# Kernel tuning notes

Measured on AMD Instinct MI355X. Metric: run time of the kernel, lower is better.

## Reference

```python
import jax, jax.numpy as jnp
import numpy as np

N_NODES = 50000
N_EDGES_UND = 400000
N_GRAPHS = 128
LATENT = 64
OUT_DIM = 64
NODE_F = 64
EDGE_F = 32
MAX_LV = 3


def setup_inputs() -> dict:
    key = jax.random.key(0)
    ks = jax.random.split(key, 12)
    rng = np.random.default_rng(0)
    # Build consistent directed edge list: each undirected pair (u,v) yields
    # directed edges e (u->v) and e+E_und (v->u); rev maps each to its twin.
    u = rng.integers(0, N_NODES, size=N_EDGES_UND)
    v = rng.integers(0, N_NODES, size=N_EDGES_UND)
    src = jnp.asarray(np.concatenate([u, v]), dtype=jnp.int32)
    dst = jnp.asarray(np.concatenate([v, u]), dtype=jnp.int32)
    e = np.arange(N_EDGES_UND)
    rev = jnp.asarray(np.concatenate([e + N_EDGES_UND, e]), dtype=jnp.int32)
    graph_ids = jnp.sort(jax.random.randint(ks[0], (N_NODES,), 0, N_GRAPHS)).astype(jnp.int32)
    s = 0.05
    return {
        'node_feat': jax.random.normal(ks[1], (N_NODES, NODE_F), jnp.float32),
        'edge_feat': jax.random.normal(ks[2], (2 * N_EDGES_UND, EDGE_F), jnp.float32),
        'src': src, 'dst': dst, 'rev': rev,
        'graph_ids': graph_ids, 'n_graphs': N_GRAPHS,
        'Wn': jax.random.normal(ks[3], (NODE_F, LATENT), jnp.float32) * s,
        'bn': jnp.zeros((LATENT,), jnp.float32),
        'We': jax.random.normal(ks[4], (EDGE_F, LATENT), jnp.float32) * s,
        'be': jnp.zeros((LATENT,), jnp.float32),
        'Wc': jax.random.normal(ks[5], (LATENT, LATENT), jnp.float32) * s,
        'bc': jnp.zeros((LATENT,), jnp.float32),
        'Wo': jax.random.normal(ks[6], (LATENT, OUT_DIM), jnp.float32) * s,
        'bo': jnp.zeros((OUT_DIM,), jnp.float32),
    }


def reference(node_feat, edge_feat, src, dst, rev, graph_ids, n_graphs,
              Wn, bn, We, be, Wc, bc, Wo, bo):
    n_nodes = node_feat.shape[0]
    # w_n2l / w_e2l
    input_node_linear = node_feat @ Wn + bn                  # [N, D]
    input_edge_linear = edge_feat @ We + be                  # [E, D]
    # n2e spmm: each directed edge gathers its source node's row
    input_message = input_edge_linear + input_node_linear[src]  # [E, D]
    cur = jax.nn.relu(input_message)
    # loopy BP: e2e spmm = (sum of messages into src node) - reverse-edge message
    for _ in range(MAX_LV):
        node_agg = jax.ops.segment_sum(cur, dst, num_segments=n_nodes)  # [N, D]
        e2epool = node_agg[src] - cur[rev]                              # [E, D]
        cur = jax.nn.relu(e2epool @ Wc + bc + input_message)
    # e2n spmm: sum incoming edge messages per node
    e2npool = jax.ops.segment_sum(cur, dst, num_segments=n_nodes)       # [N, D]
    hidden_msg = jax.nn.relu(e2npool)
    reluact = jax.nn.relu(hidden_msg @ Wo + bo)                         # [N, out]
    # subg spmm: sum node outputs per graph
    y = jax.ops.segment_sum(reluact, graph_ids, num_segments=n_graphs)  # [G, out]
    return jax.nn.relu(y)
```

## Files before the change

### kernel.cpp

```cpp
#include <hip/hip_runtime.h>


#define NN 50000
#define NE 800000
#define NG 128
#define D 64
#define LDE 36
#define LDW 66
#define LDO 72

typedef unsigned short u16;
typedef unsigned int u32;
typedef __bf16 bf16x8 __attribute__((ext_vector_type(8)));
typedef float f32x4 __attribute__((ext_vector_type(4)));

__device__ __forceinline__ float b2f(u16 u){ u32 x=((u32)u)<<16; float f; __builtin_memcpy(&f,&x,4); return f; }
__device__ __forceinline__ u16 f2b(float f){ u32 x; __builtin_memcpy(&x,&f,4); x += 0x7fffu + ((x>>16)&1u); return (u16)(x>>16); }
__device__ __forceinline__ u32 pack2(float a, float b){ return (u32)f2b(a) | ((u32)f2b(b)<<16); }
__device__ __forceinline__ void unpack8(uint4 v, float* o){
  o[0]=b2f((u16)(v.x&0xffffu)); o[1]=b2f((u16)(v.x>>16));
  o[2]=b2f((u16)(v.y&0xffffu)); o[3]=b2f((u16)(v.y>>16));
  o[4]=b2f((u16)(v.z&0xffffu)); o[5]=b2f((u16)(v.z>>16));
  o[6]=b2f((u16)(v.w&0xffffu)); o[7]=b2f((u16)(v.w>>16));
}

__global__ __launch_bounds__(256) void k_prep(const float* __restrict__ Wc, const float* __restrict__ We,
                                              u16* __restrict__ wcB, u16* __restrict__ weB){
  int i = blockIdx.x*256 + threadIdx.x;
  if (i < 4096){
    int nt = i>>10, r = i&1023;
    int h = r>>9, r2 = r&511;
    int j = r2>>3, kk = r2&7;
    int row = nt*16 + (j&15);
    int k = h*32 + (j>>4)*8 + kk;
    wcB[i] = f2b(Wc[k*D + row]);
  }
  int t = i - 4096;
  if (t >= 0 && t < 2048){
    int nt = t>>9, r = t&511;
    int j = r>>3, kk = r&7;
    int row = nt*16 + (j&15);
    int k = (j>>4)*8 + kk;
    weB[t] = f2b(We[k*D + row]);
  }
}

template<int ZERO>
__global__ __launch_bounds__(256) void k_cvt(const float* __restrict__ srcv, u16* __restrict__ dstb,
                                             float* __restrict__ zbuf){
  size_t i = (size_t)(blockIdx.x*256 + threadIdx.x)*4;
  float4 v = *(const float4*)(srcv + i);
  *(uint2*)(dstb + i) = make_uint2(pack2(v.x,v.y), pack2(v.z,v.w));
  if (ZERO) *(float4*)(zbuf + i) = make_float4(0.f,0.f,0.f,0.f);
}

__global__ __launch_bounds__(256) void k_inl(const float* __restrict__ nf, const float* __restrict__ Wn,
                                             const float* __restrict__ bn, u16* __restrict__ inlb){
  __shared__ float w[D*D];
  for (int i=threadIdx.x;i<D*D;i+=256) w[i]=Wn[i];
  __syncthreads();
  const int d = threadIdx.x&63;
  const int n = blockIdx.x*4 + (threadIdx.x>>6);
  if (n>=NN) return;
  float v = bn[d];
  const float* row = nf + (size_t)n*D;
  #pragma unroll 8
  for (int k=0;k<D;k++) v += row[k]*w[k*D+d];
  inlb[(size_t)n*D+d] = f2b(v);
}

__global__ __launch_bounds__(256) void k_imf2(const float* __restrict__ ef, const u16* __restrict__ weB,
        const float* __restrict__ be, const u16* __restrict__ inlb, const int* __restrict__ srcP,
        const int* __restrict__ eP, const int* __restrict__ nodeP, const u16* __restrict__ wcB,
        u16* __restrict__ imP, u16* __restrict__ revOut, float* __restrict__ naW_out){
  __shared__ __align__(16) u16 efs[64*LDE];
  __shared__ float osf[64*68];
  __shared__ __align__(16) u16 xs[64*LDW];
  __shared__ __align__(16) u16 osb[64*LDO];
  __shared__ int nid[64];
  const int t = threadIdx.x;
  const int lane = t&63, w = t>>6;
  const size_t sbase = (size_t)blockIdx.x*64;
  if (lane < 16) nid[w*16 + lane] = nodeP[sbase + w*16 + lane];
  {
    int r=t>>2, k0=(t&3)*8;
    const int e = eP[sbase + r];
    const float* p = ef + (size_t)e*32 + k0;
    float4 v0=*(const float4*)p, v1=*(const float4*)(p+4);
    *(uint4*)&efs[r*LDE+k0] = make_uint4(pack2(v0.x,v0.y),pack2(v0.z,v0.w),pack2(v1.x,v1.y),pack2(v1.z,v1.w));
  }
  {
    int q=lane>>4, mr=lane&15, rowb=w*16;
    bf16x8 A = *(const bf16x8*)&efs[(rowb+mr)*LDE + q*8];
    #pragma unroll
    for (int nt=0;nt<4;nt++){
      bf16x8 B = *(const bf16x8*)(weB + nt*512 + lane*8);
      f32x4 acc = {0.f,0.f,0.f,0.f};
      acc = __builtin_amdgcn_mfma_f32_16x16x32_bf16(A,B,acc,0,0,0);
      #pragma unroll
      for (int r=0;r<4;r++) osf[(rowb+q*4+r)*68 + nt*16+mr] = acc[r];
    }
  }
  {
    int r=t>>2, d0=(t&3)*16;
    const size_t slot = sbase + r;
    const int s = srcP[slot];
    const u16* ip = inlb + (size_t)s*D + d0;
    uint4 iv0 = *(const uint4*)ip, iv1 = *(const uint4*)(ip+8);
    float il[16]; unpack8(iv0,il); unpack8(iv1,il+8);
    float x[16];
    #pragma unroll
    for (int j=0;j<16;j++) x[j] = osf[r*68 + d0 + j] + be[d0+j] + il[j];
    uint4 p0 = make_uint4(pack2(x[0],x[1]),pack2(x[2],x[3]),pack2(x[4],x[5]),pack2(x[6],x[7]));
    uint4 p1 = make_uint4(pack2(x[8],x[9]),pack2(x[10],x[11]),pack2(x[12],x[13]),pack2(x[14],x[15]));
    u16* op = imP + slot*D + d0;
    *(uint4*)op = p0; *(uint4*)(op+8) = p1;
    #pragma unroll
    for (int j=0;j<16;j++) x[j] = x[j]>0.f ? x[j] : 0.f;
    uint4 q0 = make_uint4(pack2(x[0],x[1]),pack2(x[2],x[3]),pack2(x[4],x[5]),pack2(x[6],x[7]));
    uint4 q1 = make_uint4(pack2(x[8],x[9]),pack2(x[10],x[11]),pack2(x[12],x[13]),pack2(x[14],x[15]));
    u16* qd = &xs[r*LDW + d0];
    *(uint4*)qd = q0; *(uint4*)(qd+8) = q1;
  }
  {
    const int q = lane>>4, mr = lane&15;
    const int rowb = w*16;
    bf16x8 A0 = *(const bf16x8*)&xs[(rowb+mr)*LDW + q*8];
    bf16x8 A1 = *(const bf16x8*)&xs[(rowb+mr)*LDW + 32 + q*8];
    #pragma unroll
    for (int nt=0;nt<4;nt++){
      bf16x8 B0 = *(const bf16x8*)(wcB + nt*1024 + lane*8);
      bf16x8 B1 = *(const bf16x8*)(wcB + nt*1024 + 512 + lane*8);
      f32x4 acc = {0.f,0.f,0.f,0.f};
      acc = __builtin_amdgcn_mfma_f32_16x16x32_bf16(A0,B0,acc,0,0,0);
      acc = __builtin_amdgcn_mfma_f32_16x16x32_bf16(A1,B1,acc,0,0,0);
      #pragma unroll
      for (int r=0;r<4;r++) osb[(rowb+q*4+r)*LDO + nt*16 + mr] = f2b(acc[r]);
    }
    const int lr = lane>>2, cc = lane&3;
    u16* gp = revOut + (sbase + rowb + lr)*D + cc*16;
    *(uint4*)gp     = *(const uint4*)&osb[(rowb+lr)*LDO + cc*16];
    *(uint4*)(gp+8) = *(const uint4*)&osb[(rowb+lr)*LDO + cc*16 + 8];
    float acc = 0.f;
    int curn = nid[rowb];
    #pragma unroll 4
    for (int i=0;i<16;++i){
      int n = nid[rowb+i];
      if (n != curn){
        atomicAdd(&naW_out[(size_t)curn*D + lane], acc);
        curn = n; acc = 0.f;
      }
      acc += b2f(osb[(rowb+i)*LDO + lane]);
    }
    atomicAdd(&naW_out[(size_t)curn*D + lane], acc);
  }
}

__global__ __launch_bounds__(256) void k_iter1(const u16* __restrict__ imP, const u16* __restrict__ revIn,
      const u16* __restrict__ naWb, const u16* __restrict__ wcB, const float* __restrict__ bc,
      const int* __restrict__ srcP, const int* __restrict__ prevP, const int* __restrict__ nodeP,
      u16* __restrict__ revOut, float* __restrict__ naW_out){
  __shared__ __align__(16) u16 xs[64*LDW];
  __shared__ __align__(16) u16 os[64*LDO];
  __shared__ int nid[64];
  const int t = threadIdx.x;
  const int lane = t&63, w = t>>6;
  const size_t sbase = (size_t)blockIdx.x*64;
  if (lane < 16) nid[w*16 + lane] = nodeP[sbase + w*16 + lane];
  {
    const int e = t>>2, d0 = (t&3)*16;
    const size_t slot = sbase + e;
    const u16* ip = imP + slot*D + d0;
    uint4 r0 = *(const uint4*)ip, r1 = *(const uint4*)(ip+8);
    float x[16]; unpack8(r0,x); unpack8(r1,x+8);
    const int sp = srcP[slot];
    const int tw = prevP[slot];
    const u16* cp = revIn + (size_t)tw*D + d0;
    uint4 c0=*(const uint4*)cp, c1=*(const uint4*)(cp+8);
    const u16* np_ = naWb + (size_t)sp*D + d0;
    uint4 n0=*(const uint4*)np_, n1=*(const uint4*)(np_+8);
    float cv[16], nv[16];
    unpack8(c0,cv); unpack8(c1,cv+8);
    unpack8(n0,nv); unpack8(n1,nv+8);
    #pragma unroll
    for (int j=0;j<16;j++){ x[j] += nv[j] - cv[j] + bc[d0+j]; x[j] = x[j]>0.f ? x[j] : 0.f; }
    uint4 p0 = make_uint4(pack2(x[0],x[1]),pack2(x[2],x[3]),pack2(x[4],x[5]),pack2(x[6],x[7]));
    uint4 p1 = make_uint4(pack2(x[8],x[9]),pack2(x[10],x[11]),pack2(x[12],x[13]),pack2(x[14],x[15]));
    u16* qd = &xs[e*LDW + d0];
    *(uint4*)qd = p0; *(uint4*)(qd+8) = p1;
  }
  {
    const int q = lane>>4, mr = lane&15;
    const int rowb = w*16;
    bf16x8 A0 = *(const bf16x8*)&xs[(rowb+mr)*LDW + q*8];
    bf16x8 A1 = *(const bf16x8*)&xs[(rowb+mr)*LDW + 32 + q*8];
    #pragma unroll
    for (int nt=0;nt<4;nt++){
      bf16x8 B0 = *(const bf16x8*)(wcB + nt*1024 + lane*8);
      bf16x8 B1 = *(const bf16x8*)(wcB + nt*1024 + 512 + lane*8);
      f32x4 acc = {0.f,0.f,0.f,0.f};
      acc = __builtin_amdgcn_mfma_f32_16x16x32_bf16(A0,B0,acc,0,0,0);
      acc = __builtin_amdgcn_mfma_f32_16x16x32_bf16(A1,B1,acc,0,0,0);
      #pragma unroll
      for (int r=0;r<4;r++) os[(rowb+q*4+r)*LDO + nt*16 + mr] = f2b(acc[r]);
    }
    const int lr = lane>>2, cc = lane&3;
    u16* gp = revOut + (sbase + rowb + lr)*D + cc*16;
    *(uint4*)gp     = *(const uint4*)&os[(rowb+lr)*LDO + cc*16];
    *(uint4*)(gp+8) = *(const uint4*)&os[(rowb+lr)*LDO + cc*16 + 8];
    float acc = 0.f;
    int curn = nid[rowb];
    #pragma unroll 4
    for (int i=0;i<16;++i){
      int n = nid[rowb+i];
      if (n != curn){
        atomicAdd(&naW_out[(size_t)curn*D + lane], acc);
        curn = n; acc = 0.f;
      }
      acc += b2f(os[(rowb+i)*LDO + lane]);
    }
    atomicAdd(&naW_out[(size_t)curn*D + lane], acc);
  }
}

__global__ __launch_bounds__(256) void k_last(const u16* __restrict__ imP, const u16* __restrict__ revIn,
      const u16* __restrict__ naWb, const float* __restrict__ bc,
      const int* __restrict__ srcP, const int* __restrict__ prevP, const int* __restrict__ nodeP,
      float* __restrict__ e2n){
  __shared__ __align__(16) u16 xs[64*LDW];
  __shared__ int nid[64];
  const int t = threadIdx.x;
  const int lane = t&63, w = t>>6;
  const size_t sbase = (size_t)blockIdx.x*64;
  if (lane < 16) nid[w*16+lane] = nodeP[sbase + w*16 + lane];
  {
    const int e = t>>2, d0 = (t&3)*16;
    const size_t slot = sbase + e;
    const u16* ip = imP + slot*D + d0;
    uint4 r0 = *(const uint4*)ip, r1 = *(const uint4*)(ip+8);
    float x[16]; unpack8(r0,x); unpack8(r1,x+8);
    const int sp = srcP[slot];
    const int tw = prevP[slot];
    const u16* cp = revIn + (size_t)tw*D + d0;
    uint4 c0 = *(const uint4*)cp, c1 = *(const uint4*)(cp+8);
    const u16* np_ = naWb + (size_t)sp*D + d0;
    uint4 n0 = *(const uint4*)np_, n1 = *(const uint4*)(np_+8);
    float cv[16], nv[16];
    unpack8(c0,cv); unpack8(c1,cv+8);
    unpack8(n0,nv); unpack8(n1,nv+8);
    #pragma unroll
    for (int j=0;j<16;j++){ x[j] += nv[j] - cv[j] + bc[d0+j]; x[j] = x[j]>0.f ? x[j] : 0.f; }
    uint4 p0 = make_uint4(pack2(x[0],x[1]),pack2(x[2],x[3]),pack2(x[4],x[5]),pack2(x[6],x[7]));
    uint4 p1 = make_uint4(pack2(x[8],x[9]),pack2(x[10],x[11]),pack2(x[12],x[13]),pack2(x[14],x[15]));
    u16* qd = &xs[e*LDW + d0];
    *(uint4*)qd = p0; *(uint4*)(qd+8) = p1;
  }
  {
    float acc = 0.f;
    int curn = nid[w*16];
    #pragma unroll 4
    for (int i=0;i<16;++i){
      int n = nid[w*16+i];
      if (n != curn){
        atomicAdd(&e2n[(size_t)curn*D + lane], acc);
        curn = n; acc = 0.f;
      }
      acc += b2f(xs[(w*16+i)*LDW + lane]);
    }
    atomicAdd(&e2n[(size_t)curn*D + lane], acc);
  }
}

__global__ void k_hist(const int* __restrict__ dst, int* __restrict__ cnt){
  int e = blockIdx.x*256 + threadIdx.x;
  atomicAdd(&cnt[dst[e]], 1);
}
__global__ __launch_bounds__(1024) void k_scan1(const int* __restrict__ cnt, int* __restrict__ outv,
                                                int* __restrict__ bsums, int n){
  __shared__ int sh[1024];
  int i = blockIdx.x*1024 + threadIdx.x;
  int v = (i<n)? cnt[i] : 0;
  sh[threadIdx.x]=v;
  __syncthreads();
  for (int off=1; off<1024; off<<=1){
    int tv = (threadIdx.x>=(unsigned)off)? sh[threadIdx.x-off] : 0;
    __syncthreads();
    sh[threadIdx.x] += tv;
    __syncthreads();
  }
  if (i<n) outv[i] = sh[threadIdx.x] - v;
  if (threadIdx.x==1023) bsums[blockIdx.x] = sh[1023];
}
__global__ __launch_bounds__(1024) void k_scan3(int* __restrict__ off, int* __restrict__ cur,
                                                const int* __restrict__ bsums, int n){
  __shared__ int spref;
  if (threadIdx.x < 64){
    int v = ((int)threadIdx.x < (int)blockIdx.x) ? bsums[threadIdx.x] : 0;
    #pragma unroll
    for (int o=1;o<64;o<<=1) v += __shfl_xor(v, o, 64);
    if (threadIdx.x==0) spref = v;
  }
  __syncthreads();
  int i = blockIdx.x*1024 + threadIdx.x;
  if (i<n){ int v = off[i] + spref; off[i]=v; cur[i]=v; }
}
__global__ void k_fill(const int* __restrict__ dst, const int* __restrict__ src,
                       int* __restrict__ cur, int* __restrict__ perm,
                       int* __restrict__ srcP, int* __restrict__ nodeP, int* __restrict__ eP){
  int e = blockIdx.x*256 + threadIdx.x;
  int d = dst[e];
  int pos = atomicAdd(&cur[d], 1);
  perm[e] = pos;
  srcP[pos] = src[e];
  nodeP[pos] = d;
  eP[pos] = e;
}
__global__ void k_prev(const int* __restrict__ rev, const int* __restrict__ perm, int* __restrict__ prevP){
  int e = blockIdx.x*256 + threadIdx.x;
  prevP[perm[e]] = perm[rev[e]];
}

__global__ __launch_bounds__(256) void k_final(const float* __restrict__ e2n, const float* __restrict__ Wo,
                                               const float* __restrict__ bo, const int* __restrict__ gid,
                                               float* __restrict__ yacc){
  __shared__ float w[D*D];
  for (int i=threadIdx.x;i<D*D;i+=256) w[i]=Wo[i];
  __syncthreads();
  const int d = threadIdx.x&63, sub = threadIdx.x>>6;
  const int n0 = blockIdx.x*32 + sub*8;
  const float bod = bo[d];
  float acc=0.f; int curg=-1;
  for (int i=0;i<8;i++){
    int n=n0+i;
    if (n>=NN) break;
    int g = gid[n];
    if (g!=curg){ if (curg>=0) atomicAdd(&yacc[curg*D+d], acc); curg=g; acc=0.f; }
    float v=bod;
    const float* er = e2n + (size_t)n*D;
    #pragma unroll 8
    for (int k=0;k<D;k++){ float h=er[k]; h = h>0.f?h:0.f; v += h*w[k*D+d]; }
    acc += (v>0.f ? v : 0.f);
  }
  if (curg>=0) atomicAdd(&yacc[curg*D+d], acc);
}
__global__ void k_out(const float* __restrict__ yacc, float* __restrict__ outp){
  int i = blockIdx.x*256 + threadIdx.x;
  if (i<NG*D){ float v=yacc[i]; outp[i]= v>0.f?v:0.f; }
}

static constexpr size_t SZ_E   = (size_t)NE*D*2;
static constexpr size_t SZ_NF4 = (size_t)NN*D*4;
static constexpr size_t SZ_NB  = (size_t)NN*D*2;
static constexpr size_t OFF_IMP  = 0;
static constexpr size_t OFF_RVA  = SZ_E;
static constexpr size_t OFF_RVB  = 2*SZ_E;
static constexpr size_t OFF_CCUR = 3*SZ_E;
static constexpr size_t OFF_NA0  = OFF_CCUR + 200064;
static constexpr size_t OFF_NA1  = OFF_NA0 + SZ_NF4;
static constexpr size_t OFF_E2N  = OFF_NA1 + SZ_NF4;
static constexpr size_t OFF_YACC = OFF_E2N + SZ_NF4;
static constexpr size_t ZERO_SZ  = 200064 + 3*SZ_NF4 + (size_t)NG*D*4;
static constexpr size_t OFF_NAB  = OFF_YACC + (size_t)NG*D*4;
static constexpr size_t OFF_INL  = OFF_NAB + SZ_NB;
static constexpr size_t OFF_COFF = OFF_INL + SZ_NB;
static constexpr size_t OFF_PERM = OFF_COFF + 200064;
static constexpr size_t OFF_SRCP = OFF_PERM + (size_t)NE*4;
static constexpr size_t OFF_PRVP = OFF_SRCP + (size_t)NE*4;
static constexpr size_t OFF_NODP = OFF_PRVP + (size_t)NE*4;
static constexpr size_t OFF_EP   = OFF_NODP + (size_t)NE*4;
static constexpr size_t OFF_BS   = OFF_EP + (size_t)NE*4;
static constexpr size_t OFF_WCT  = OFF_BS + 256;
static constexpr size_t OFF_WET  = OFF_WCT + 8192;

extern "C" void kernel_launch(void* const* d_in, const int* in_sizes, int n_in,
                              void* d_out, int out_size, void* d_ws, size_t ws_size,
                              hipStream_t stream) {
  const float* node_feat = (const float*)d_in[0];
  const float* edge_feat = (const float*)d_in[1];
  const int*   src       = (const int*)d_in[2];
  const int*   dst       = (const int*)d_in[3];
  const int*   rev       = (const int*)d_in[4];
  const int*   gid       = (const int*)d_in[5];
  const float* Wn = (const float*)d_in[7];
  const float* bn = (const float*)d_in[8];
  const float* We = (const float*)d_in[9];
  const float* be = (const float*)d_in[10];
  const float* Wc = (const float*)d_in[11];
  const float* bc = (const float*)d_in[12];
  const float* Wo = (const float*)d_in[13];
  const float* bo = (const float*)d_in[14];

  char* ws = (char*)d_ws;
  u16*   imP     = (u16*)(ws + OFF_IMP);
  u16*   revA    = (u16*)(ws + OFF_RVA);
  u16*   revB    = (u16*)(ws + OFF_RVB);
  float* naW0    = (float*)(ws + OFF_NA0);
  float* naW1    = (float*)(ws + OFF_NA1);
  float* e2n     = (float*)(ws + OFF_E2N);
  float* yacc    = (float*)(ws + OFF_YACC);
  u16*   naWb    = (u16*)(ws + OFF_NAB);
  u16*   inlb    = (u16*)(ws + OFF_INL);
  int*   csr_off = (int*)(ws + OFF_COFF);
  int*   csr_cur = (int*)(ws + OFF_CCUR);
  int*   perm    = (int*)(ws + OFF_PERM);
  int*   srcP    = (int*)(ws + OFF_SRCP);
  int*   prevP   = (int*)(ws + OFF_PRVP);
  int*   nodeP   = (int*)(ws + OFF_NODP);
  int*   eP      = (int*)(ws + OFF_EP);
  int*   bsums   = (int*)(ws + OFF_BS);
  u16*   wcB     = (u16*)(ws + OFF_WCT);
  u16*   weB     = (u16*)(ws + OFF_WET);

  hipMemsetAsync(ws + OFF_CCUR, 0, ZERO_SZ, stream);

  k_hist <<<NE/256, 256, 0, stream>>>(dst, csr_cur);
  k_scan1<<<49, 1024, 0, stream>>>(csr_cur, csr_off, bsums, NN);
  k_scan3<<<49, 1024, 0, stream>>>(csr_off, csr_cur, bsums, NN);
  k_fill <<<NE/256, 256, 0, stream>>>(dst, src, csr_cur, perm, srcP, nodeP, eP);
  k_prev <<<NE/256, 256, 0, stream>>>(rev, perm, prevP);

  k_prep<<<24, 256, 0, stream>>>(Wc, We, wcB, weB);
  k_inl <<<NN/4, 256, 0, stream>>>(node_feat, Wn, bn, inlb);

  k_imf2<<<NE/64, 256, 0, stream>>>(edge_feat, weB, be, inlb, srcP, eP, nodeP, wcB, imP, revA, naW0);

  k_cvt<0><<<3125, 256, 0, stream>>>(naW0, naWb, (float*)nullptr);
  k_iter1<<<NE/64, 256, 0, stream>>>(imP, revA, naWb, wcB, bc, srcP, prevP, nodeP, revB, naW1);
  k_cvt<1><<<3125, 256, 0, stream>>>(naW1, naWb, naW0);
  k_iter1<<<NE/64, 256, 0, stream>>>(imP, revB, naWb, wcB, bc, srcP, prevP, nodeP, revA, naW0);
  k_cvt<0><<<3125, 256, 0, stream>>>(naW0, naWb, (float*)nullptr);
  k_last<<<NE/64, 256, 0, stream>>>(imP, revA, naWb, bc, srcP, prevP, nodeP, e2n);

  k_final<<<(NN+31)/32, 256, 0, stream>>>(e2n, Wo, bo, gid, yacc);
  k_out<<<(NG*D)/256, 256, 0, stream>>>(yacc, (float*)d_out);
}
```

Before: 697.3 us.

## Scatter reverse-edge messages at write time so consumers read them coalesced

Each producer kernel now writes its per-edge Wc-projected message to the reverse edge's slot via prevP, so the next iteration reads revIn at its own slot with coalesced loads instead of a random gather. The random access moves from the read side to the write side, where stores can be fire-and-forget. k_imf2 also packs its shared buffers into per-wave aliased regions to cut LDS use and raise occupancy. The risk is that scattered 32-byte stores are less efficient than coalesced ones.

```diff
diff --git a/kernel.cpp b/kernel.cpp
--- a/kernel.cpp
+++ b/kernel.cpp
@@ -8,6 +8,7 @@
 #define LDE 36
 #define LDW 66
 #define LDO 72
+#define PW 6464
 
 typedef unsigned short u16;
 typedef unsigned int u32;
@@ -71,38 +72,41 @@
 
 __global__ __launch_bounds__(256) void k_imf2(const float* __restrict__ ef, const u16* __restrict__ weB,
         const float* __restrict__ be, const u16* __restrict__ inlb, const int* __restrict__ srcP,
-        const int* __restrict__ eP, const int* __restrict__ nodeP, const u16* __restrict__ wcB,
+        const int* __restrict__ eP, const int* __restrict__ nodeP, const int* __restrict__ prevP,
+        const u16* __restrict__ wcB,
         u16* __restrict__ imP, u16* __restrict__ revOut, float* __restrict__ naW_out){
-  __shared__ __align__(16) u16 efs[64*LDE];
-  __shared__ float osf[64*68];
-  __shared__ __align__(16) u16 xs[64*LDW];
-  __shared__ __align__(16) u16 osb[64*LDO];
+  __shared__ __align__(16) char buf[4*PW];
   __shared__ int nid[64];
   const int t = threadIdx.x;
   const int lane = t&63, w = t>>6;
   const size_t sbase = (size_t)blockIdx.x*64;
+  char* wb = buf + w*PW;
+  float* osf = (float*)wb;
+  u16*   osb = (u16*)wb;
+  u16*   efs = (u16*)(wb + 4352);
+  u16*   xs  = (u16*)(wb + 4352);
   if (lane < 16) nid[w*16 + lane] = nodeP[sbase + w*16 + lane];
   {
-    int r=t>>2, k0=(t&3)*8;
+    int r=t>>2, lr=r&15, k0=(t&3)*8;
     const int e = eP[sbase + r];
     const float* p = ef + (size_t)e*32 + k0;
     float4 v0=*(const float4*)p, v1=*(const float4*)(p+4);
-    *(uint4*)&efs[r*LDE+k0] = make_uint4(pack2(v0.x,v0.y),pack2(v0.z,v0.w),pack2(v1.x,v1.y),pack2(v1.z,v1.w));
-  }
-  {
-    int q=lane>>4, mr=lane&15, rowb=w*16;
-    bf16x8 A = *(const bf16x8*)&efs[(rowb+mr)*LDE + q*8];
+    *(uint4*)&efs[lr*LDE+k0] = make_uint4(pack2(v0.x,v0.y),pack2(v0.z,v0.w),pack2(v1.x,v1.y),pack2(v1.z,v1.w));
+  }
+  {
+    int q=lane>>4, mr=lane&15;
+    bf16x8 A = *(const bf16x8*)&efs[mr*LDE + q*8];
     #pragma unroll
     for (int nt=0;nt<4;nt++){
       bf16x8 B = *(const bf16x8*)(weB + nt*512 + lane*8);
       f32x4 acc = {0.f,0.f,0.f,0.f};
       acc = __builtin_amdgcn_mfma_f32_16x16x32_bf16(A,B,acc,0,0,0);
       #pragma unroll
-      for (int r=0;r<4;r++) osf[(rowb+q*4+r)*68 + nt*16+mr] = acc[r];
-    }
-  }
-  {
-    int r=t>>2, d0=(t&3)*16;
+      for (int r=0;r<4;r++) osf[(q*4+r)*68 + nt*16+mr] = acc[r];
+    }
+  }
+  {
+    int r=t>>2, lr=r&15, d0=(t&3)*16;
     const size_t slot = sbase + r;
     const int s = srcP[slot];
     const u16* ip = inlb + (size_t)s*D + d0;
@@ -110,7 +114,7 @@
     float il[16]; unpack8(iv0,il); unpack8(iv1,il+8);
     float x[16];
     #pragma unroll
-    for (int j=0;j<16;j++) x[j] = osf[r*68 + d0 + j] + be[d0+j] + il[j];
+    for (int j=0;j<16;j++) x[j] = osf[lr*68 + d0 + j] + be[d0+j] + il[j];
     uint4 p0 = make_uint4(pack2(x[0],x[1]),pack2(x[2],x[3]),pack2(x[4],x[5]),pack2(x[6],x[7]));
     uint4 p1 = make_uint4(pack2(x[8],x[9]),pack2(x[10],x[11]),pack2(x[12],x[13]),pack2(x[14],x[15]));
     u16* op = imP + slot*D + d0;
@@ -119,14 +123,13 @@
     for (int j=0;j<16;j++) x[j] = x[j]>0.f ? x[j] : 0.f;
     uint4 q0 = make_uint4(pack2(x[0],x[1]),pack2(x[2],x[3]),pack2(x[4],x[5]),pack2(x[6],x[7]));
     uint4 q1 = make_uint4(pack2(x[8],x[9]),pack2(x[10],x[11]),pack2(x[12],x[13]),pack2(x[14],x[15]));
-    u16* qd = &xs[r*LDW + d0];
+    u16* qd = &xs[lr*LDW + d0];
     *(uint4*)qd = q0; *(uint4*)(qd+8) = q1;
   }
   {
     const int q = lane>>4, mr = lane&15;
-    const int rowb = w*16;
-    bf16x8 A0 = *(const bf16x8*)&xs[(rowb+mr)*LDW + q*8];
-    bf16x8 A1 = *(const bf16x8*)&xs[(rowb+mr)*LDW + 32 + q*8];
+    bf16x8 A0 = *(const bf16x8*)&xs[mr*LDW + q*8];
+    bf16x8 A1 = *(const bf16x8*)&xs[mr*LDW + 32 + q*8];
     #pragma unroll
     for (int nt=0;nt<4;nt++){
       bf16x8 B0 = *(const bf16x8*)(wcB + nt*1024 + lane*8);
@@ -135,22 +138,23 @@
       acc = __builtin_amdgcn_mfma_f32_16x16x32_bf16(A0,B0,acc,0,0,0);
       acc = __builtin_amdgcn_mfma_f32_16x16x32_bf16(A1,B1,acc,0,0,0);
       #pragma unroll
-      for (int r=0;r<4;r++) osb[(rowb+q*4+r)*LDO + nt*16 + mr] = f2b(acc[r]);
+      for (int r=0;r<4;r++) osb[(q*4+r)*LDO + nt*16 + mr] = f2b(acc[r]);
     }
     const int lr = lane>>2, cc = lane&3;
-    u16* gp = revOut + (sbase + rowb + lr)*D + cc*16;
-    *(uint4*)gp     = *(const uint4*)&osb[(rowb+lr)*LDO + cc*16];
-    *(uint4*)(gp+8) = *(const uint4*)&osb[(rowb+lr)*LDO + cc*16 + 8];
+    const int tgt = prevP[sbase + w*16 + lr];
+    u16* gp = revOut + (size_t)tgt*D + cc*16;
+    *(uint4*)gp     = *(const uint4*)&osb[lr*LDO + cc*16];
+    *(uint4*)(gp+8) = *(const uint4*)&osb[lr*LDO + cc*16 + 8];
     float acc = 0.f;
-    int curn = nid[rowb];
+    int curn = nid[w*16];
     #pragma unroll 4
     for (int i=0;i<16;++i){
-      int n = nid[rowb+i];
+      int n = nid[w*16+i];
       if (n != curn){
         atomicAdd(&naW_out[(size_t)curn*D + lane], acc);
         curn = n; acc = 0.f;
       }
-      acc += b2f(osb[(rowb+i)*LDO + lane]);
+      acc += b2f(osb[i*LDO + lane]);
     }
     atomicAdd(&naW_out[(size_t)curn*D + lane], acc);
   }
@@ -174,8 +178,7 @@
     uint4 r0 = *(const uint4*)ip, r1 = *(const uint4*)(ip+8);
     float x[16]; unpack8(r0,x); unpack8(r1,x+8);
     const int sp = srcP[slot];
-    const int tw = prevP[slot];
-    const u16* cp = revIn + (size_t)tw*D + d0;
+    const u16* cp = revIn + slot*D + d0;
     uint4 c0=*(const uint4*)cp, c1=*(const uint4*)(cp+8);
     const u16* np_ = naWb + (size_t)sp*D + d0;
     uint4 n0=*(const uint4*)np_, n1=*(const uint4*)(np_+8);
@@ -205,7 +208,8 @@
       for (int r=0;r<4;r++) os[(rowb+q*4+r)*LDO + nt*16 + mr] = f2b(acc[r]);
     }
     const int lr = lane>>2, cc = lane&3;
-    u16* gp = revOut + (sbase + rowb + lr)*D + cc*16;
+    const int tgt = prevP[sbase + rowb + lr];
+    u16* gp = revOut + (size_t)tgt*D + cc*16;
     *(uint4*)gp     = *(const uint4*)&os[(rowb+lr)*LDO + cc*16];
     *(uint4*)(gp+8) = *(const uint4*)&os[(rowb+lr)*LDO + cc*16 + 8];
     float acc = 0.f;
@@ -225,7 +229,7 @@
 
 __global__ __launch_bounds__(256) void k_last(const u16* __restrict__ imP, const u16* __restrict__ revIn,
       const u16* __restrict__ naWb, const float* __restrict__ bc,
-      const int* __restrict__ srcP, const int* __restrict__ prevP, const int* __restrict__ nodeP,
+      const int* __restrict__ srcP, const int* __restrict__ nodeP,
       float* __restrict__ e2n){
   __shared__ __align__(16) u16 xs[64*LDW];
   __shared__ int nid[64];
@@ -240,8 +244,7 @@
     uint4 r0 = *(const uint4*)ip, r1 = *(const uint4*)(ip+8);
     float x[16]; unpack8(r0,x); unpack8(r1,x+8);
     const int sp = srcP[slot];
-    const int tw = prevP[slot];
-    const u16* cp = revIn + (size_t)tw*D + d0;
+    const u16* cp = revIn + slot*D + d0;
     uint4 c0 = *(const uint4*)cp, c1 = *(const uint4*)(cp+8);
     const u16* np_ = naWb + (size_t)sp*D + d0;
     uint4 n0 = *(const uint4*)np_, n1 = *(const uint4*)(np_+8);
@@ -422,14 +425,14 @@
   k_prep<<<24, 256, 0, stream>>>(Wc, We, wcB, weB);
   k_inl <<<NN/4, 256, 0, stream>>>(node_feat, Wn, bn, inlb);
 
-  k_imf2<<<NE/64, 256, 0, stream>>>(edge_feat, weB, be, inlb, srcP, eP, nodeP, wcB, imP, revA, naW0);
+  k_imf2<<<NE/64, 256, 0, stream>>>(edge_feat, weB, be, inlb, srcP, eP, nodeP, prevP, wcB, imP, revA, naW0);
 
   k_cvt<0><<<3125, 256, 0, stream>>>(naW0, naWb, (float*)nullptr);
   k_iter1<<<NE/64, 256, 0, stream>>>(imP, revA, naWb, wcB, bc, srcP, prevP, nodeP, revB, naW1);
   k_cvt<1><<<3125, 256, 0, stream>>>(naW1, naWb, naW0);
   k_iter1<<<NE/64, 256, 0, stream>>>(imP, revB, naWb, wcB, bc, srcP, prevP, nodeP, revA, naW0);
   k_cvt<0><<<3125, 256, 0, stream>>>(naW0, naWb, (float*)nullptr);
-  k_last<<<NE/64, 256, 0, stream>>>(imP, revA, naWb, bc, srcP, prevP, nodeP, e2n);
+  k_last<<<NE/64, 256, 0, stream>>>(imP, revA, naWb, bc, srcP, nodeP, e2n);
 
   k_final<<<(NN+31)/32, 256, 0, stream>>>(e2n, Wo, bo, gid, yacc);
   k_out<<<(NG*D)/256, 256, 0, stream>>>(yacc, (float*)d_out);
```

Result: no change. 691.4 us (-0.8%).
